# Kernel tuning notes

Measured on AMD Instinct MI355X. Metric: run time of the kernel, lower is better.

Reference implementation:

```python
import jax, jax.numpy as jnp
import numpy as np

FRAMESIZE = 80


def setup_inputs() -> dict:
    key = jax.random.key(0)
    k1, k2 = jax.random.split(key)
    B, t, nbands = 32, 4000, 257
    H = jax.random.normal(k1, (B, t, nbands), dtype=jnp.float32)
    noise_u = jax.random.uniform(k2, (B, t, FRAMESIZE), dtype=jnp.float32)
    return {"H": H, "noise_u": noise_u}


def reference(H, noise_u):
    """Time-varying filtered noise via linear-phase LTV-FIR + overlap-add.

    H       : [B, t, nbands] half spectrum (real) of zero-phase filter
    noise_u : [B, t, framesize] uniform noise in [0, 1)
    returns : [B, t*framesize]
    """
    framesize = FRAMESIZE
    B, t, nbands = H.shape
    N = 2 * nbands - 1  # FIR length L (odd)

    # torch.hann_window default is periodic: w[n] = 0.5*(1 - cos(2*pi*n/N))
    hann = (0.5 * (1.0 - jnp.cos(2.0 * jnp.pi * jnp.arange(N) / N))).astype(jnp.float32)

    # zero-phase impulse response -> linear phase via circular shift, then window
    zero_phase = jnp.fft.irfft(H, n=N, axis=-1)              # [B, t, N]
    lin_phase = jnp.roll(zero_phase, nbands - 1, axis=-1)    # [B, t, N]
    firwin = lin_phase * hann                                # [B, t, N]
    L = N

    noise = noise_u * 2.0 - 1.0                              # uniform in [-1, 1)

    # full linear convolution per (B, t) frame via FFT (fftconvolve, mode='full')
    nfft = framesize + L - 1
    Fn = jnp.fft.rfft(noise, n=nfft, axis=-1)
    Ff = jnp.fft.rfft(firwin, n=nfft, axis=-1)
    filtered = jnp.fft.irfft(Fn * Ff, n=nfft, axis=-1)       # [B, t, framesize+L-1]

    # overlap-add with hop = framesize (the conv_transpose1d(eye) trick, done as
    # a direct strided scatter-add), then trim the L-1 tail as in the original
    out_len = t * framesize + L - 1
    idx = (jnp.arange(t)[:, None] * framesize + jnp.arange(nfft)[None, :]).reshape(-1)
    out = jnp.zeros((B, out_len), dtype=filtered.dtype)
    out = out.at[:, idx].add(filtered.reshape(B, -1))
    return out[:, : t * framesize]
```

## Files before the change

kernel.cpp:

```cpp
#include <hip/hip_runtime.h>
#include <stdint.h>

typedef unsigned short u16;
typedef unsigned int   u32;
typedef __attribute__((ext_vector_type(8))) short short8;
typedef __attribute__((ext_vector_type(4))) float f32x4;

#define TPB 256
#define FPB 64
#define NB 257
#define LF 513
#define FS 80
#define NCH 9
#define MT_TOTAL 33
#define HROW 296
#define FROW 536
#define TAB_ELEMS (MT_TOTAL*NCH*64*8)

__device__ __forceinline__ u32 f2bf(float f){
  u32 u = __float_as_uint(f);
  return (u + 0x7fffu + ((u >> 16) & 1u)) >> 16;
}
#define BF2LO(u) __uint_as_float((u) << 16)
#define BF2HI(u) __uint_as_float((u) & 0xffff0000u)

__global__ void build_table(u16* __restrict__ tab){
  int id = blockIdx.x * blockDim.x + threadIdx.x;
  if (id >= TAB_ELEMS) return;
  int j    = id & 7;
  int lane = (id >> 3) & 63;
  int cc   = (id >> 9) % NCH;
  int mt   = (id >> 9) / NCH;
  int tap  = mt * 16 + (lane & 15);
  int kslot= cc * 32 + (lane >> 4) * 8 + j;
  float val = 0.f;
  if (tap < LF){
    float hann = 0.5f - 0.5f * cosf(6.28318530717958647f * (float)tap / 513.f);
    if (kslot < 256){
      int k  = kslot + 1;
      int rr = (k * (tap + 257)) % 513;
      val = (2.f / 513.f) * hann * cosf((float)rr * (6.28318530717958647f / 513.f));
    } else if (kslot == 256){
      val = hann * (1.f / 513.f);
    }
  }
  tab[id] = (u16)f2bf(val);
}

__launch_bounds__(TPB, 2)
__global__ void fused(const float* __restrict__ Hg, const float* __restrict__ noiseg,
                      const u16* __restrict__ tab, float* __restrict__ out, int outTotal){
  __shared__ u16 uSh[FPB * FROW];
  __shared__ u16 noiseSh[FPB * FS];

  const int tid  = threadIdx.x;
  const int lane = tid & 63;
  const int w    = tid >> 6;
  const int ln15 = lane & 15;
  const int q    = lane >> 4;
  const int blk  = blockIdx.x;
  const int f0   = blk * FPB;

  u16* Hlds = uSh;

  #pragma unroll
  for (int e = 0; e < 32; ++e){
    int id = tid + TPB * e;
    int r = id >> 7, p = id & 127;
    const float* gp = Hg + (size_t)(f0 + r) * NB + 1 + 2 * p;
    u32 lo = f2bf(gp[0]), hi = f2bf(gp[1]);
    *(u32*)&Hlds[r * HROW + 2 * p] = lo | (hi << 16);
  }
  if (tid < 64){
    *(u32*)&Hlds[tid * HROW + 256] = f2bf(Hg[(size_t)(f0 + tid) * NB]);
  }
  #pragma unroll
  for (int e = 0; e < 5; ++e){
    int id = tid + TPB * e;
    if (id < 64 * 19){
      int r = id / 19, c2 = id % 19;
      *(u32*)&Hlds[r * HROW + 258 + 2 * c2] = 0u;
    }
  }
  #pragma unroll
  for (int e = 0; e < 10; ++e){
    int id = tid + TPB * e;
    int r = id / 40, c2 = id % 40;
    float2 v = *(const float2*)(noiseg + (size_t)(f0 + r) * FS + 2 * c2);
    u32 lo = f2bf(v.x * 2.f - 1.f), hi = f2bf(v.y * 2.f - 1.f);
    *(u32*)&noiseSh[r * FS + 2 * c2] = lo | (hi << 16);
  }
  __syncthreads();

  const int mtBegin = (w == 0) ? 0 : (9 + 8 * (w - 1));
  const int mtCount = (w == 0) ? 9 : 8;
  f32x4 acc[9][4];
  #pragma unroll
  for (int a = 0; a < 9; ++a)
    #pragma unroll
    for (int b = 0; b < 4; ++b) acc[a][b] = (f32x4){0.f, 0.f, 0.f, 0.f};

  const short8* tab8 = (const short8*)tab;
  for (int c = 0; c < NCH; ++c){
    short8 bfrag[4];
    #pragma unroll
    for (int nt = 0; nt < 4; ++nt)
      bfrag[nt] = *(const short8*)&Hlds[(nt * 16 + ln15) * HROW + c * 32 + q * 8];
    #pragma unroll
    for (int mt = 0; mt < 9; ++mt){
      if (mt < mtCount){
        short8 afrag = tab8[((mtBegin + mt) * NCH + c) * 64 + lane];
        #pragma unroll
        for (int nt = 0; nt < 4; ++nt)
          acc[mt][nt] = __builtin_amdgcn_mfma_f32_16x16x32_bf16(afrag, bfrag[nt], acc[mt][nt], 0, 0, 0);
      }
    }
  }
  __syncthreads();

  u16* fir = uSh;
  #pragma unroll
  for (int mt = 0; mt < 9; ++mt){
    if (mt < mtCount){
      int tap0 = (mtBegin + mt) * 16 + q * 4;
      #pragma unroll
      for (int nt = 0; nt < 4; ++nt){
        int frame = nt * 16 + ln15;
        f32x4 v = acc[mt][nt];
        uint2 pk;
        pk.x = f2bf(v.x) | (f2bf(v.y) << 16);
        pk.y = f2bf(v.z) | (f2bf(v.w) << 16);
        *(uint2*)&fir[frame * FROW + 8 + tap0] = pk;
      }
    }
  }
  if (tid < 256){
    int r = tid >> 2, s = tid & 3;
    ((u32*)&fir[r * FROW])[s] = 0u;
  }
  __syncthreads();

  for (int task = tid; task < 704; task += TPB){
    int s0 = blk * (FPB * FS) + task * 8;
    if (s0 >= outTotal) continue;
    int qb = s0 / 320000;
    int fA = max(f0, qb * 4000);
    int fB = min(f0 + FPB, qb * 4000 + 4000);
    int fLo = max(fA, (s0 >= 512) ? (s0 - 512) / 80 : 0);
    int fHi = min(fB - 1, (s0 + 7) / 80);
    float ac[8];
    #pragma unroll
    for (int r = 0; r < 8; ++r) ac[r] = 0.f;

    for (int f = fLo; f <= fHi; ++f){
      int frel = f - f0;
      int j0 = s0 - 80 * f;
      const u16* frow = uSh + frel * FROW + 8;
      const u16* nrow = noiseSh + frel * FS;
      int gLo = (j0 > 512) ? ((j0 - 512) >> 2) : 0;
      int gHi = min(19, (j0 >> 2) + 1);
      float F[12];
      int x = j0 - 4 * gLo;
      uint2 q1 = *(const uint2*)(frow + x);
      uint2 q2 = *(const uint2*)(frow + x + 4);
      F[4] = BF2LO(q1.x); F[5] = BF2HI(q1.x); F[6]  = BF2LO(q1.y); F[7]  = BF2HI(q1.y);
      F[8] = BF2LO(q2.x); F[9] = BF2HI(q2.x); F[10] = BF2LO(q2.y); F[11] = BF2HI(q2.y);
      for (int g = gLo; g <= gHi; ++g){
        uint2 q0 = *(const uint2*)(frow + (j0 - 4 * g - 4));
        F[0] = BF2LO(q0.x); F[1] = BF2HI(q0.x); F[2] = BF2LO(q0.y); F[3] = BF2HI(q0.y);
        uint2 nq = *(const uint2*)(nrow + 4 * g);
        float n0 = BF2LO(nq.x), n1 = BF2HI(nq.x), n2 = BF2LO(nq.y), n3 = BF2HI(nq.y);
        #pragma unroll
        for (int r = 0; r < 8; ++r){
          ac[r] = fmaf(n0, F[4 + r], ac[r]);
          ac[r] = fmaf(n1, F[3 + r], ac[r]);
          ac[r] = fmaf(n2, F[2 + r], ac[r]);
          ac[r] = fmaf(n3, F[1 + r], ac[r]);
        }
        F[8] = F[4]; F[9] = F[5]; F[10] = F[6]; F[11] = F[7];
        F[4] = F[0]; F[5] = F[1]; F[6]  = F[2]; F[7]  = F[3];
      }
    }
    if (task >= 64 && task < 640){
      float4 v0 = make_float4(ac[0], ac[1], ac[2], ac[3]);
      float4 v1 = make_float4(ac[4], ac[5], ac[6], ac[7]);
      *(float4*)&out[s0]     = v0;
      *(float4*)&out[s0 + 4] = v1;
    } else if (fLo <= fHi){
      #pragma unroll
      for (int r = 0; r < 8; ++r) atomicAdd(&out[s0 + r], ac[r]);
    }
  }
}

extern "C" void kernel_launch(void* const* d_in, const int* in_sizes, int n_in,
                              void* d_out, int out_size, void* d_ws, size_t ws_size,
                              hipStream_t stream){
  const float* Hg     = (const float*)d_in[0];
  const float* noiseg = (const float*)d_in[1];
  float* out = (float*)d_out;
  u16* tab = (u16*)d_ws;

  hipMemsetAsync(d_out, 0, (size_t)out_size * sizeof(float), stream);
  build_table<<<TAB_ELEMS / TPB, TPB, 0, stream>>>(tab);
  fused<<<(32 * 4000) / FPB, TPB, 0, stream>>>(Hg, noiseg, tab, out, out_size);
}
```

Before: 557.9 us.

## Remap overlap-add tasks so lanes share offsets, pad LDS rows against bank conflicts

Restructures the overlap-add phase so that each wavefront handles one within-frame offset (t0) and each lane one frame. All lanes in a wave then run identical loop bounds and identical j0 offsets, which removes divergence from per-task variable frame ranges. The tail tasks that spill into the next block are moved to a separate path on wave 3 that uses atomics. FIR and noise LDS rows are padded (540/84) to change bank mapping for the now-strided per-lane row accesses. The risk is load imbalance between waves, since waves 0-1 take 3 offsets and waves 2-3 take 2 plus the tail.

```diff
diff --git a/kernel.cpp b/kernel.cpp
--- a/kernel.cpp
+++ b/kernel.cpp
@@ -14,7 +14,8 @@
 #define NCH 9
 #define MT_TOTAL 33
 #define HROW 296
-#define FROW 536
+#define FROW 540
+#define NROW 84
 #define TAB_ELEMS (MT_TOTAL*NCH*64*8)
 
 __device__ __forceinline__ u32 f2bf(float f){
@@ -47,11 +48,37 @@
   tab[id] = (u16)f2bf(val);
 }
 
+__device__ __forceinline__ void convFrame(const u16* frow, const u16* nrow, int j0, float ac[8]){
+  int gLo = (j0 > 512) ? ((j0 - 512) >> 2) : 0;
+  int gHi = min(19, (j0 >> 2) + 1);
+  float F[12];
+  int x = j0 - 4 * gLo;
+  uint2 q1 = *(const uint2*)(frow + x);
+  uint2 q2 = *(const uint2*)(frow + x + 4);
+  F[4] = BF2LO(q1.x); F[5] = BF2HI(q1.x); F[6]  = BF2LO(q1.y); F[7]  = BF2HI(q1.y);
+  F[8] = BF2LO(q2.x); F[9] = BF2HI(q2.x); F[10] = BF2LO(q2.y); F[11] = BF2HI(q2.y);
+  for (int g = gLo; g <= gHi; ++g){
+    uint2 q0 = *(const uint2*)(frow + (j0 - 4 * g - 4));
+    F[0] = BF2LO(q0.x); F[1] = BF2HI(q0.x); F[2] = BF2LO(q0.y); F[3] = BF2HI(q0.y);
+    uint2 nq = *(const uint2*)(nrow + 4 * g);
+    float n0 = BF2LO(nq.x), n1 = BF2HI(nq.x), n2 = BF2LO(nq.y), n3 = BF2HI(nq.y);
+    #pragma unroll
+    for (int r = 0; r < 8; ++r){
+      ac[r] = fmaf(n0, F[4 + r], ac[r]);
+      ac[r] = fmaf(n1, F[3 + r], ac[r]);
+      ac[r] = fmaf(n2, F[2 + r], ac[r]);
+      ac[r] = fmaf(n3, F[1 + r], ac[r]);
+    }
+    F[8] = F[4]; F[9] = F[5]; F[10] = F[6]; F[11] = F[7];
+    F[4] = F[0]; F[5] = F[1]; F[6]  = F[2]; F[7]  = F[3];
+  }
+}
+
 __launch_bounds__(TPB, 2)
 __global__ void fused(const float* __restrict__ Hg, const float* __restrict__ noiseg,
                       const u16* __restrict__ tab, float* __restrict__ out, int outTotal){
   __shared__ u16 uSh[FPB * FROW];
-  __shared__ u16 noiseSh[FPB * FS];
+  __shared__ u16 noiseSh[FPB * NROW];
 
   const int tid  = threadIdx.x;
   const int lane = tid & 63;
@@ -88,7 +115,7 @@
     int r = id / 40, c2 = id % 40;
     float2 v = *(const float2*)(noiseg + (size_t)(f0 + r) * FS + 2 * c2);
     u32 lo = f2bf(v.x * 2.f - 1.f), hi = f2bf(v.y * 2.f - 1.f);
-    *(u32*)&noiseSh[r * FS + 2 * c2] = lo | (hi << 16);
+    *(u32*)&noiseSh[r * NROW + 2 * c2] = lo | (hi << 16);
   }
   __syncthreads();
 
@@ -140,55 +167,53 @@
   }
   __syncthreads();
 
-  for (int task = tid; task < 704; task += TPB){
-    int s0 = blk * (FPB * FS) + task * 8;
-    if (s0 >= outTotal) continue;
-    int qb = s0 / 320000;
-    int fA = max(f0, qb * 4000);
-    int fB = min(f0 + FPB, qb * 4000 + 4000);
-    int fLo = max(fA, (s0 >= 512) ? (s0 - 512) / 80 : 0);
-    int fHi = min(fB - 1, (s0 + 7) / 80);
+  const int base = blk * (FPB * FS);
+  for (int t0 = w; t0 < 10; t0 += 4){
+    const int task = t0 + 10 * lane;
+    const int s0 = base + task * 8;
+    const int qb = s0 / 320000;
+    const int rLo = max(0, qb * 4000 - f0);
+    const int rHi = min(FPB, qb * 4000 + 4000 - f0);
     float ac[8];
     #pragma unroll
     for (int r = 0; r < 8; ++r) ac[r] = 0.f;
 
-    for (int f = fLo; f <= fHi; ++f){
-      int frel = f - f0;
-      int j0 = s0 - 80 * f;
-      const u16* frow = uSh + frel * FROW + 8;
-      const u16* nrow = noiseSh + frel * FS;
-      int gLo = (j0 > 512) ? ((j0 - 512) >> 2) : 0;
-      int gHi = min(19, (j0 >> 2) + 1);
-      float F[12];
-      int x = j0 - 4 * gLo;
-      uint2 q1 = *(const uint2*)(frow + x);
-      uint2 q2 = *(const uint2*)(frow + x + 4);
-      F[4] = BF2LO(q1.x); F[5] = BF2HI(q1.x); F[6]  = BF2LO(q1.y); F[7]  = BF2HI(q1.y);
-      F[8] = BF2LO(q2.x); F[9] = BF2HI(q2.x); F[10] = BF2LO(q2.y); F[11] = BF2HI(q2.y);
-      for (int g = gLo; g <= gHi; ++g){
-        uint2 q0 = *(const uint2*)(frow + (j0 - 4 * g - 4));
-        F[0] = BF2LO(q0.x); F[1] = BF2HI(q0.x); F[2] = BF2LO(q0.y); F[3] = BF2HI(q0.y);
-        uint2 nq = *(const uint2*)(nrow + 4 * g);
-        float n0 = BF2LO(nq.x), n1 = BF2HI(nq.x), n2 = BF2LO(nq.y), n3 = BF2HI(nq.y);
-        #pragma unroll
-        for (int r = 0; r < 8; ++r){
-          ac[r] = fmaf(n0, F[4 + r], ac[r]);
-          ac[r] = fmaf(n1, F[3 + r], ac[r]);
-          ac[r] = fmaf(n2, F[2 + r], ac[r]);
-          ac[r] = fmaf(n3, F[1 + r], ac[r]);
-        }
-        F[8] = F[4]; F[9] = F[5]; F[10] = F[6]; F[11] = F[7];
-        F[4] = F[0]; F[5] = F[1]; F[6]  = F[2]; F[7]  = F[3];
-      }
-    }
-    if (task >= 64 && task < 640){
-      float4 v0 = make_float4(ac[0], ac[1], ac[2], ac[3]);
-      float4 v1 = make_float4(ac[4], ac[5], ac[6], ac[7]);
-      *(float4*)&out[s0]     = v0;
-      *(float4*)&out[s0 + 4] = v1;
-    } else if (fLo <= fHi){
+    const int dMax = (t0 >= 4) ? 6 : 7;
+    for (int d = 0; d <= dMax; ++d){
+      const int frel = lane - d;
+      const int j0 = 8 * t0 + 80 * d;
+      if (frel >= rLo && frel < rHi){
+        convFrame(uSh + frel * FROW + 8, noiseSh + frel * NROW, j0, ac);
+      }
+    }
+    if (task >= 64){
+      *(float4*)&out[s0]     = make_float4(ac[0], ac[1], ac[2], ac[3]);
+      *(float4*)&out[s0 + 4] = make_float4(ac[4], ac[5], ac[6], ac[7]);
+    } else {
       #pragma unroll
       for (int r = 0; r < 8; ++r) atomicAdd(&out[s0 + r], ac[r]);
+    }
+  }
+
+  if (w == 3){
+    const int task = 640 + lane;
+    const int s0 = base + task * 8;
+    if (s0 < outTotal){
+      const int qb = s0 / 320000;
+      const int fA = max(f0, qb * 4000);
+      const int fB = min(f0 + FPB, qb * 4000 + 4000);
+      const int fLo = max(fA, (s0 - 512) / 80);
+      const int fHi = min(fB - 1, (s0 + 7) / 80);
+      float ac[8];
+      #pragma unroll
+      for (int r = 0; r < 8; ++r) ac[r] = 0.f;
+      for (int f = fLo; f <= fHi; ++f){
+        convFrame(uSh + (f - f0) * FROW + 8, noiseSh + (f - f0) * NROW, s0 - 80 * f, ac);
+      }
+      if (fLo <= fHi){
+        #pragma unroll
+        for (int r = 0; r < 8; ++r) atomicAdd(&out[s0 + r], ac[r]);
+      }
     }
   }
 }
```

Result: faster. 528.6 us (-5.2%).
